# Performance work log

Hardware: AMD Instinct MI355X
Metric: run time of the kernel (lower is better)

Reference implementation:

```python
import jax, jax.numpy as jnp
import numpy as np
import math

B, N, C = 8, 2048, 512

def setup_inputs() -> dict:
    key = jax.random.key(0)
    ks = jax.random.split(key, 7)
    s = 1.0 / math.sqrt(C)
    return {
        "feature": jax.random.normal(ks[0], (B, N, C), dtype=jnp.float32),
        "wq": jax.random.uniform(ks[1], (C, C), jnp.float32, -s, s),
        "bq": jax.random.uniform(ks[2], (C,), jnp.float32, -s, s),
        "wk": jax.random.uniform(ks[3], (C, C), jnp.float32, -s, s),
        "bk": jax.random.uniform(ks[4], (C,), jnp.float32, -s, s),
        "wv": jax.random.uniform(ks[5], (C, C), jnp.float32, -s, s),
        "bv": jax.random.uniform(ks[6], (C,), jnp.float32, -s, s),
    }

def reference(feature, wq, bq, wk, bk, wv, bv):
    # torch nn.Linear: x @ W.T + b
    q = jnp.einsum('bnc,dc->bnd', feature, wq) + bq
    k = jnp.einsum('bnc,dc->bnd', feature, wk) + bk
    v = jnp.einsum('bnc,dc->bnd', feature, wv) + bv
    scores = jnp.einsum('bnd,bmd->bnm', q, k)          # [B, N, N]
    attn = jax.nn.softmax(scores, axis=2) / math.sqrt(C)  # post-softmax scale (as in source)
    v_star = jnp.einsum('bnm,bmd->bnd', attn, v)
    return feature + v_star
```

## Files before the change

### kernel.cpp

```cpp
#include <hip/hip_runtime.h>
#include <cstdint>
#include <cstddef>


typedef __bf16 bf16x8 __attribute__((ext_vector_type(8)));
typedef float f32x4 __attribute__((ext_vector_type(4)));
typedef float f32x16 __attribute__((ext_vector_type(16)));
typedef short short4v __attribute__((ext_vector_type(4)));
typedef short short8v __attribute__((ext_vector_type(8)));

__device__ __forceinline__ short f2b(float f) {
  union { float f; unsigned u; } u; u.f = f;
  unsigned r = (u.u + 0x7fffu + ((u.u >> 16) & 1u)) >> 16;
  return (short)r;
}

#define GLDS(gptr, lptr) \
  __builtin_amdgcn_global_load_lds( \
      (const __attribute__((address_space(1))) unsigned int*)(const void*)(gptr), \
      (__attribute__((address_space(3))) unsigned int*)(void*)(lptr), 16, 0, 0)

__device__ __forceinline__ bf16x8 ldfrag64(const short* buf, int row, int kq) {
  return *(const bf16x8*)(buf + row * 64 + ((kq ^ (row & 7)) * 8));
}

__global__ __launch_bounds__(256) void prep(const float* __restrict__ f,
                                            const float* __restrict__ w0,
                                            const float* __restrict__ w1,
                                            const float* __restrict__ w2,
                                            const float* __restrict__ b0,
                                            const float* __restrict__ b1,
                                            const float* __restrict__ b2,
                                            short* __restrict__ Xb, short* __restrict__ Wb,
                                            float* __restrict__ biasP, float* __restrict__ l) {
  const int bid = blockIdx.x;
  const int t = threadIdx.x;
  if (bid < 8192) {
    int i = bid * 256 + t;
    float4 v = ((const float4*)f)[i];
    short4v o = { f2b(v.x), f2b(v.y), f2b(v.z), f2b(v.w) };
    *(short4v*)(Xb + (size_t)i * 4) = o;
  } else if (bid < 8960) {
    int i = (bid - 8192) * 256 + t;
    const float* src = (i < 65536) ? w0 : (i < 131072) ? w1 : w2;
    float4 v = ((const float4*)src)[i & 65535];
    short4v o = { f2b(v.x), f2b(v.y), f2b(v.z), f2b(v.w) };
    *(short4v*)(Wb + (size_t)i * 4) = o;
  } else {
    int i = (bid - 8960) * 256 + t;
    float4 z = { 0.f, 0.f, 0.f, 0.f };
    ((float4*)l)[i * 2] = z;
    ((float4*)l)[i * 2 + 1] = z;
    if (i < 1536) {
      const float* s = (i < 512) ? b0 : (i < 1024) ? b1 : b2;
      biasP[i] = s[i & 511];
    }
  }
}

__global__ __launch_bounds__(256) void gemm_qkv(const short* __restrict__ X,
                                                const short* __restrict__ Wall,
                                                const float* __restrict__ biasP,
                                                short* __restrict__ Out,
                                                short* __restrict__ VtOut) {
  __shared__ __align__(16) short Xs[128 * 64];
  __shared__ __align__(16) short Ws[128 * 64];
  const int z = blockIdx.z;
  const short* Wm = Wall + (size_t)z * 262144;
  const int m0 = blockIdx.y * 128, n0 = blockIdx.x * 128;
  const int t = threadIdx.x;
  const int lane = t & 63, w = t >> 6;
  const int wn = (w & 1) * 64, wm = (w >> 1) * 64;
  const int fr = lane & 15, l4 = lane >> 4;

  f32x4 acc[4][4] = {};

  for (int k0 = 0; k0 < 512; k0 += 64) {
    __syncthreads();
#pragma unroll
    for (int u = 0; u < 4; ++u) {
      int cc = t + u * 256;
      int r = cc >> 3, cs = cc & 7;
      int kk = ((cs ^ (r & 7)) * 8);
      GLDS(X + (size_t)(m0 + r) * 512 + k0 + kk, Xs + cc * 8);
      GLDS(Wm + (size_t)(n0 + r) * 512 + k0 + kk, Ws + cc * 8);
    }
    __syncthreads();
#pragma unroll
    for (int h = 0; h < 2; ++h) {
      bf16x8 wf[4], xf[4];
#pragma unroll
      for (int i = 0; i < 4; ++i) wf[i] = ldfrag64(Ws, wn + i * 16 + fr, h * 4 + l4);
#pragma unroll
      for (int j = 0; j < 4; ++j) xf[j] = ldfrag64(Xs, wm + j * 16 + fr, h * 4 + l4);
      if (z < 2) {
#pragma unroll
        for (int i = 0; i < 4; ++i)
#pragma unroll
          for (int j = 0; j < 4; ++j)
            acc[i][j] = __builtin_amdgcn_mfma_f32_16x16x32_bf16(wf[i], xf[j], acc[i][j], 0, 0, 0);
      } else {
#pragma unroll
        for (int i = 0; i < 4; ++i)
#pragma unroll
          for (int j = 0; j < 4; ++j)
            acc[i][j] = __builtin_amdgcn_mfma_f32_16x16x32_bf16(xf[i], wf[j], acc[i][j], 0, 0, 0);
      }
    }
  }

  const int rq = l4 * 4;
  if (z < 2) {
#pragma unroll
    for (int i = 0; i < 4; ++i) {
      int nb = n0 + wn + i * 16 + rq;
      float4 bs = *(const float4*)(biasP + z * 512 + nb);
#pragma unroll
      for (int j = 0; j < 4; ++j) {
        int m = m0 + wm + j * 16 + fr;
        short4v o = { f2b(acc[i][j][0] + bs.x), f2b(acc[i][j][1] + bs.y),
                      f2b(acc[i][j][2] + bs.z), f2b(acc[i][j][3] + bs.w) };
        *(short4v*)(Out + (size_t)z * 8388608 + (size_t)m * 512 + nb) = o;
      }
    }
  } else {
    const int zB = blockIdx.y >> 4;
    const int mb = m0 & 2047;
#pragma unroll
    for (int j = 0; j < 4; ++j) {
      int d = n0 + wn + j * 16 + fr;
      float bd = biasP[1024 + d];
#pragma unroll
      for (int i = 0; i < 4; ++i) {
        int mloc = mb + wm + i * 16 + rq;
        short4v o = { f2b(acc[i][j][0] + bd), f2b(acc[i][j][1] + bd),
                      f2b(acc[i][j][2] + bd), f2b(acc[i][j][3] + bd) };
        *(short4v*)(VtOut + (size_t)zB * 1048576 + (size_t)d * 2048 + mloc) = o;
      }
    }
  }
}

__global__ __launch_bounds__(256) void gemm_qk(const short* __restrict__ Q,
                                               const short* __restrict__ Kb,
                                               short* __restrict__ P,
                                               float* __restrict__ l) {
  __shared__ __align__(16) short Qs[128 * 64];
  __shared__ __align__(16) short Ks[128 * 64];
  const int z = blockIdx.z;
  const short* A = Q + (size_t)z * 2048 * 512;
  const short* Bm = Kb + (size_t)z * 2048 * 512;
  const int m0 = blockIdx.y * 128, n0 = blockIdx.x * 128;
  const int t = threadIdx.x;
  const int lane = t & 63, w = t >> 6;
  const int wn = (w & 1) * 64, wm = (w >> 1) * 64;
  const int c31 = lane & 31, l5 = lane >> 5;

  f32x16 acc[2][2] = {};

  for (int k0 = 0; k0 < 512; k0 += 64) {
    __syncthreads();
#pragma unroll
    for (int u = 0; u < 4; ++u) {
      int cc = t + u * 256;
      int r = cc >> 3, cs = cc & 7;
      int kk = ((cs ^ (r & 7)) * 8);
      GLDS(A + (size_t)(m0 + r) * 512 + k0 + kk, Qs + cc * 8);
      GLDS(Bm + (size_t)(n0 + r) * 512 + k0 + kk, Ks + cc * 8);
    }
    __syncthreads();
#pragma unroll
    for (int ks = 0; ks < 4; ++ks) {
      const int kq = ks * 2 + l5;
      bf16x8 kf[2], qf[2];
#pragma unroll
      for (int i = 0; i < 2; ++i) kf[i] = ldfrag64(Ks, wn + i * 32 + c31, kq);
#pragma unroll
      for (int j = 0; j < 2; ++j) qf[j] = ldfrag64(Qs, wm + j * 32 + c31, kq);
#pragma unroll
      for (int i = 0; i < 2; ++i)
#pragma unroll
        for (int j = 0; j < 2; ++j)
          acc[i][j] = __builtin_amdgcn_mfma_f32_32x32x16_bf16(kf[i], qf[j], acc[i][j], 0, 0, 0);
    }
  }

  float rs[2] = { 0.f, 0.f };
#pragma unroll
  for (int i = 0; i < 2; ++i)
#pragma unroll
    for (int q = 0; q < 4; ++q) {
      int nb = n0 + wn + i * 32 + q * 8 + l5 * 4;
#pragma unroll
      for (int j = 0; j < 2; ++j) {
        int m = m0 + wm + j * 32 + c31;
        short4v o;
        float part = 0.f;
#pragma unroll
        for (int r = 0; r < 4; ++r) {
          float e = exp2f(acc[i][j][q * 4 + r] * 1.4426950408889634f);
          o[r] = f2b(e);
          part += e;
        }
        *(short4v*)(P + (size_t)z * 4194304 + (size_t)m * 2048 + nb) = o;
        rs[j] += part;
      }
    }
#pragma unroll
  for (int j = 0; j < 2; ++j) rs[j] += __shfl_xor(rs[j], 32);
  if (lane < 32) {
#pragma unroll
    for (int j = 0; j < 2; ++j)
      atomicAdd(&l[z * 2048 + m0 + wm + j * 32 + lane], rs[j]);
  }
}

__global__ __launch_bounds__(256) void gemm_pv(const short* __restrict__ Pm,
                                               const short* __restrict__ Vt,
                                               const float* __restrict__ l,
                                               const float* __restrict__ resid,
                                               float* __restrict__ out, float scale) {
  __shared__ __align__(16) short Ps[64 * 64];
  __shared__ __align__(16) short Vs[2][128 * 64];
  const int z = blockIdx.z;
  const short* A = Pm + (size_t)z * 4194304;
  const short* Bm = Vt + (size_t)z * 1048576;
  const int m0 = blockIdx.y * 64, n0 = blockIdx.x * 256;
  const int t = threadIdx.x;
  const int lane = t & 63, w = t >> 6;
  const int wn = (w & 1) * 64, wm = (w >> 1) * 32;
  const int c31 = lane & 31, l5 = lane >> 5;

  f32x16 acc[2][2] = {};

  for (int k0 = 0; k0 < 2048; k0 += 64) {
    __syncthreads();
#pragma unroll
    for (int u = 0; u < 2; ++u) {
      int cc = t + u * 256;
      int r = cc >> 3, cs = cc & 7;
      int kk = ((cs ^ (r & 7)) * 8);
      GLDS(A + (size_t)(m0 + r) * 2048 + k0 + kk, Ps + cc * 8);
    }
#pragma unroll
    for (int nt = 0; nt < 2; ++nt)
#pragma unroll
      for (int u = 0; u < 4; ++u) {
        int cc = t + u * 256;
        int r = cc >> 3, cs = cc & 7;
        int kk = ((cs ^ (r & 7)) * 8);
        GLDS(Bm + (size_t)(n0 + nt * 128 + r) * 2048 + k0 + kk, Vs[nt] + cc * 8);
      }
    __syncthreads();
#pragma unroll
    for (int ks = 0; ks < 4; ++ks) {
      const int kq = ks * 2 + l5;
      bf16x8 pf = ldfrag64(Ps, wm + c31, kq);
#pragma unroll
      for (int nt = 0; nt < 2; ++nt)
#pragma unroll
        for (int i = 0; i < 2; ++i) {
          bf16x8 vf = ldfrag64(Vs[nt], wn + i * 32 + c31, kq);
          acc[nt][i] = __builtin_amdgcn_mfma_f32_32x32x16_bf16(vf, pf, acc[nt][i], 0, 0, 0);
        }
    }
  }

  const int m = m0 + wm + c31;
  const float linv = scale / l[z * 2048 + m];
#pragma unroll
  for (int nt = 0; nt < 2; ++nt)
#pragma unroll
    for (int i = 0; i < 2; ++i)
#pragma unroll
      for (int q = 0; q < 4; ++q) {
        int d = n0 + nt * 128 + wn + i * 32 + q * 8 + l5 * 4;
        size_t idx = (size_t)z * 1048576 + (size_t)m * 512 + d;
        float4 rv = *(const float4*)(resid + idx);
        float4 o = { rv.x + acc[nt][i][q * 4 + 0] * linv, rv.y + acc[nt][i][q * 4 + 1] * linv,
                     rv.z + acc[nt][i][q * 4 + 2] * linv, rv.w + acc[nt][i][q * 4 + 3] * linv };
        *(float4*)(out + idx) = o;
      }
}

extern "C" void kernel_launch(void* const* d_in, const int* in_sizes, int n_in,
                              void* d_out, int out_size, void* d_ws, size_t ws_size,
                              hipStream_t stream) {
  const float* feature = (const float*)d_in[0];
  const float* wq = (const float*)d_in[1];
  const float* bq = (const float*)d_in[2];
  const float* wk = (const float*)d_in[3];
  const float* bk = (const float*)d_in[4];
  const float* wv = (const float*)d_in[5];
  const float* bv = (const float*)d_in[6];
  float* out = (float*)d_out;

  const size_t MN = (size_t)16384 * 512;
  short* Xb = (short*)d_ws;
  short* Wb = Xb + MN;
  short* Q = Wb + 786432;
  short* K = Q + MN;
  short* Vt = K + MN;
  short* P = Vt + MN;
  float* biasP = (float*)(P + (size_t)8 * 2048 * 2048);
  float* l = biasP + 1536;

  prep<<<8968, 256, 0, stream>>>(feature, wq, wk, wv, bq, bk, bv, Xb, Wb, biasP, l);

  gemm_qkv<<<dim3(4, 128, 3), 256, 0, stream>>>(Xb, Wb, biasP, Q, Vt);
  gemm_qk<<<dim3(16, 16, 8), 256, 0, stream>>>(Q, K, P, l);

  const float iscl = 0.044194173824159216f;
  gemm_pv<<<dim3(2, 32, 8), 256, 0, stream>>>(P, Vt, l, feature, out, iscl);
}
```

Baseline: 250.4 us.

## Rewrite QK and PV GEMMs as 8-wave 256-tiles with pipelined LDS loads

Replaces the QK^T and PV kernels with 512-thread versions that use 256x256 (QK) and 128x256 (PV) output tiles and 16x16x32 MFMA instructions. Global-to-LDS loads are double-buffered and interleaved with four compute phases per k-step, using explicit vmcnt waits, barriers and setprio. The intent is to hide global memory latency and raise data reuse per block, at the cost of more LDS per block and fragile hand-tuned wait counts. Operand roles are swapped so that keys and Vt form the A side.

Result: no change. 250.5 us (+0.0%).

```diff
diff --git a/kernel.cpp b/kernel.cpp
--- a/kernel.cpp
+++ b/kernel.cpp
@@ -5,9 +5,7 @@
 
 typedef __bf16 bf16x8 __attribute__((ext_vector_type(8)));
 typedef float f32x4 __attribute__((ext_vector_type(4)));
-typedef float f32x16 __attribute__((ext_vector_type(16)));
 typedef short short4v __attribute__((ext_vector_type(4)));
-typedef short short8v __attribute__((ext_vector_type(8)));
 
 __device__ __forceinline__ short f2b(float f) {
   union { float f; unsigned u; } u; u.f = f;
@@ -22,6 +20,53 @@
 
 __device__ __forceinline__ bf16x8 ldfrag64(const short* buf, int row, int kq) {
   return *(const bf16x8*)(buf + row * 64 + ((kq ^ (row & 7)) * 8));
+}
+
+template <int VM>
+__device__ __forceinline__ void ph_mid() {
+  if constexpr (VM >= 0) asm volatile("s_waitcnt vmcnt(%0)" ::"n"(VM) : "memory");
+  __builtin_amdgcn_s_barrier();
+  __builtin_amdgcn_s_setprio(1);
+}
+__device__ __forceinline__ void ph_end() {
+  __builtin_amdgcn_s_setprio(0);
+  __builtin_amdgcn_s_barrier();
+  __builtin_amdgcn_sched_barrier(0);
+}
+
+__device__ __forceinline__ void ldA4(bf16x8 (&a)[4][2], const short* buf, int rb, int l4) {
+#pragma unroll
+  for (int j = 0; j < 4; ++j)
+#pragma unroll
+    for (int kk = 0; kk < 2; ++kk) a[j][kk] = ldfrag64(buf, rb + j * 16, kk * 4 + l4);
+}
+__device__ __forceinline__ void ld2(bf16x8 (&b)[2][2], const short* buf, int rb, int l4) {
+#pragma unroll
+  for (int n = 0; n < 2; ++n)
+#pragma unroll
+    for (int kk = 0; kk < 2; ++kk) b[n][kk] = ldfrag64(buf, rb + n * 16, kk * 4 + l4);
+}
+__device__ __forceinline__ void mm42(f32x4 (&acc)[8][4], const bf16x8 (&a)[4][2],
+                                     const bf16x8 (&b)[2][2], int io, int no) {
+#pragma unroll
+  for (int j = 0; j < 4; ++j)
+#pragma unroll
+    for (int n = 0; n < 2; ++n)
+#pragma unroll
+      for (int kk = 0; kk < 2; ++kk)
+        acc[io + j][no + n] = __builtin_amdgcn_mfma_f32_16x16x32_bf16(
+            a[j][kk], b[n][kk], acc[io + j][no + n], 0, 0, 0);
+}
+__device__ __forceinline__ void mm22(f32x4 (&acc)[4][4], const bf16x8 (&a)[2][2],
+                                     const bf16x8 (&b)[2][2], int io, int no) {
+#pragma unroll
+  for (int j = 0; j < 2; ++j)
+#pragma unroll
+    for (int n = 0; n < 2; ++n)
+#pragma unroll
+      for (int kk = 0; kk < 2; ++kk)
+        acc[io + j][no + n] = __builtin_amdgcn_mfma_f32_16x16x32_bf16(
+            a[j][kk], b[n][kk], acc[io + j][no + n], 0, 0, 0);
 }
 
 __global__ __launch_bounds__(256) void prep(const float* __restrict__ f,
@@ -141,146 +186,212 @@
   }
 }
 
-__global__ __launch_bounds__(256) void gemm_qk(const short* __restrict__ Q,
-                                               const short* __restrict__ Kb,
-                                               short* __restrict__ P,
-                                               float* __restrict__ l) {
-  __shared__ __align__(16) short Qs[128 * 64];
-  __shared__ __align__(16) short Ks[128 * 64];
+__global__ __launch_bounds__(512, 2) void gemm_qk8(const short* __restrict__ Q,
+                                                   const short* __restrict__ Kb,
+                                                   short* __restrict__ P,
+                                                   float* __restrict__ l) {
+  __shared__ __align__(16) short As[2][16384];
+  __shared__ __align__(16) short Bs[2][16384];
   const int z = blockIdx.z;
-  const short* A = Q + (size_t)z * 2048 * 512;
-  const short* Bm = Kb + (size_t)z * 2048 * 512;
-  const int m0 = blockIdx.y * 128, n0 = blockIdx.x * 128;
+  const short* __restrict__ A = Kb + (size_t)z * 1048576;
+  const short* __restrict__ B = Q + (size_t)z * 1048576;
+  const int m0 = blockIdx.y * 256;
+  const int n0 = blockIdx.x * 256;
   const int t = threadIdx.x;
   const int lane = t & 63, w = t >> 6;
-  const int wn = (w & 1) * 64, wm = (w >> 1) * 64;
-  const int c31 = lane & 31, l5 = lane >> 5;
-
-  f32x16 acc[2][2] = {};
-
-  for (int k0 = 0; k0 < 512; k0 += 64) {
-    __syncthreads();
-#pragma unroll
-    for (int u = 0; u < 4; ++u) {
-      int cc = t + u * 256;
-      int r = cc >> 3, cs = cc & 7;
-      int kk = ((cs ^ (r & 7)) * 8);
-      GLDS(A + (size_t)(m0 + r) * 512 + k0 + kk, Qs + cc * 8);
-      GLDS(Bm + (size_t)(n0 + r) * 512 + k0 + kk, Ks + cc * 8);
-    }
-    __syncthreads();
-#pragma unroll
-    for (int ks = 0; ks < 4; ++ks) {
-      const int kq = ks * 2 + l5;
-      bf16x8 kf[2], qf[2];
-#pragma unroll
-      for (int i = 0; i < 2; ++i) kf[i] = ldfrag64(Ks, wn + i * 32 + c31, kq);
-#pragma unroll
-      for (int j = 0; j < 2; ++j) qf[j] = ldfrag64(Qs, wm + j * 32 + c31, kq);
-#pragma unroll
-      for (int i = 0; i < 2; ++i)
-#pragma unroll
-        for (int j = 0; j < 2; ++j)
-          acc[i][j] = __builtin_amdgcn_mfma_f32_32x32x16_bf16(kf[i], qf[j], acc[i][j], 0, 0, 0);
-    }
-  }
-
-  float rs[2] = { 0.f, 0.f };
-#pragma unroll
-  for (int i = 0; i < 2; ++i)
-#pragma unroll
-    for (int q = 0; q < 4; ++q) {
-      int nb = n0 + wn + i * 32 + q * 8 + l5 * 4;
-#pragma unroll
-      for (int j = 0; j < 2; ++j) {
-        int m = m0 + wm + j * 32 + c31;
-        short4v o;
-        float part = 0.f;
-#pragma unroll
-        for (int r = 0; r < 4; ++r) {
-          float e = exp2f(acc[i][j][q * 4 + r] * 1.4426950408889634f);
-          o[r] = f2b(e);
-          part += e;
-        }
-        *(short4v*)(P + (size_t)z * 4194304 + (size_t)m * 2048 + nb) = o;
-        rs[j] += part;
+  const int aw = (w >> 2) * 64, bw = (w & 3) * 32;
+  const int fr = lane & 15, l4 = lane >> 4;
+  const int r0 = t >> 3;
+  const int kswz = ((t & 7) ^ (r0 & 7)) * 8;
+  const short* pA = A + (size_t)(m0 + r0) * 512 + kswz;
+  const short* pB = B + (size_t)(n0 + r0) * 512 + kswz;
+
+#define QK_STG_A(buf, h, kt) do { \
+    GLDS(pA + (size_t)((h) * 128) * 512 + (kt) * 64, &As[(buf)][(h) * 8192 + t * 8]); \
+    GLDS(pA + (size_t)((h) * 128 + 64) * 512 + (kt) * 64, &As[(buf)][(h) * 8192 + 4096 + t * 8]); \
+  } while (0)
+#define QK_STG_B(buf, h, kt) do { \
+    GLDS(pB + (size_t)((h) * 128) * 512 + (kt) * 64, &Bs[(buf)][(h) * 8192 + t * 8]); \
+    GLDS(pB + (size_t)((h) * 128 + 64) * 512 + (kt) * 64, &Bs[(buf)][(h) * 8192 + 4096 + t * 8]); \
+  } while (0)
+
+  f32x4 acc[8][4] = {};
+
+  QK_STG_A(0, 0, 0); QK_STG_B(0, 0, 0); QK_STG_B(0, 1, 0); QK_STG_A(0, 1, 0);
+  QK_STG_A(1, 0, 1); QK_STG_B(1, 0, 1); QK_STG_B(1, 1, 1);
+  asm volatile("s_waitcnt vmcnt(10)" ::: "memory");
+  __builtin_amdgcn_s_barrier();
+  __builtin_amdgcn_sched_barrier(0);
+
+  bf16x8 af[4][2], b0[2][2], b1[2][2];
+  for (int kt = 0; kt < 6; ++kt) {
+    const int c = kt & 1;
+    const short* Ac = &As[c][0];
+    const short* Bc = &Bs[c][0];
+    ldA4(af, Ac, aw + fr, l4); ld2(b0, Bc, bw + fr, l4);
+    QK_STG_A(c ^ 1, 1, kt + 1);
+    ph_mid<10>(); mm42(acc, af, b0, 0, 0); ph_end();
+    ld2(b1, Bc, 128 + bw + fr, l4);
+    QK_STG_A(c, 0, kt + 2);
+    ph_mid<10>(); mm42(acc, af, b1, 0, 2); ph_end();
+    ldA4(af, Ac, 128 + aw + fr, l4);
+    QK_STG_B(c, 0, kt + 2);
+    ph_mid<-1>(); mm42(acc, af, b1, 4, 2); ph_end();
+    QK_STG_B(c, 1, kt + 2);
+    ph_mid<10>(); mm42(acc, af, b0, 4, 0); ph_end();
+  }
+  {
+    const short *Ac = &As[0][0], *Bc = &Bs[0][0];
+    ldA4(af, Ac, aw + fr, l4); ld2(b0, Bc, bw + fr, l4);
+    QK_STG_A(1, 1, 7);
+    ph_mid<10>(); mm42(acc, af, b0, 0, 0); ph_end();
+    ld2(b1, Bc, 128 + bw + fr, l4);
+    ph_mid<8>();  mm42(acc, af, b1, 0, 2); ph_end();
+    ldA4(af, Ac, 128 + aw + fr, l4);
+    ph_mid<-1>(); mm42(acc, af, b1, 4, 2); ph_end();
+    ph_mid<4>();  mm42(acc, af, b0, 4, 0); ph_end();
+  }
+  {
+    const short *Ac = &As[1][0], *Bc = &Bs[1][0];
+    ldA4(af, Ac, aw + fr, l4); ld2(b0, Bc, bw + fr, l4);
+    ph_mid<2>();  mm42(acc, af, b0, 0, 0); ph_end();
+    ld2(b1, Bc, 128 + bw + fr, l4);
+    ph_mid<0>();  mm42(acc, af, b1, 0, 2); ph_end();
+    ldA4(af, Ac, 128 + aw + fr, l4);
+    ph_mid<-1>(); mm42(acc, af, b1, 4, 2); ph_end();
+    ph_mid<-1>(); mm42(acc, af, b0, 4, 0); ph_end();
+  }
+#undef QK_STG_A
+#undef QK_STG_B
+
+  const float LOG2E = 1.4426950408889634f;
+  float rs[4] = { 0.f, 0.f, 0.f, 0.f };
+#pragma unroll
+  for (int i = 0; i < 8; ++i) {
+    const int key = m0 + aw + (i & 3) * 16 + (i >> 2) * 128 + l4 * 4;
+#pragma unroll
+    for (int n = 0; n < 4; ++n) {
+      const int q = n0 + bw + (n & 1) * 16 + (n >> 1) * 128 + fr;
+      short4v o;
+      float part = 0.f;
+#pragma unroll
+      for (int r = 0; r < 4; ++r) {
+        float e = exp2f(acc[i][n][r] * LOG2E);
+        o[r] = f2b(e);
+        part += e;
       }
-    }
-#pragma unroll
-  for (int j = 0; j < 2; ++j) rs[j] += __shfl_xor(rs[j], 32);
-  if (lane < 32) {
-#pragma unroll
-    for (int j = 0; j < 2; ++j)
-      atomicAdd(&l[z * 2048 + m0 + wm + j * 32 + lane], rs[j]);
-  }
-}
-
-__global__ __launch_bounds__(256) void gemm_pv(const short* __restrict__ Pm,
-                                               const short* __restrict__ Vt,
-                                               const float* __restrict__ l,
-                                               const float* __restrict__ resid,
-                                               float* __restrict__ out, float scale) {
-  __shared__ __align__(16) short Ps[64 * 64];
-  __shared__ __align__(16) short Vs[2][128 * 64];
+      *(short4v*)(P + (size_t)z * 4194304 + (size_t)q * 2048 + key) = o;
+      rs[n] += part;
+    }
+  }
+#pragma unroll
+  for (int n = 0; n < 4; ++n) {
+    rs[n] += __shfl_xor(rs[n], 16);
+    rs[n] += __shfl_xor(rs[n], 32);
+  }
+  if (l4 == 0) {
+#pragma unroll
+    for (int n = 0; n < 4; ++n)
+      atomicAdd(&l[z * 2048 + n0 + bw + (n & 1) * 16 + (n >> 1) * 128 + fr], rs[n]);
+  }
+}
+
+__global__ __launch_bounds__(512, 2) void gemm_pv8(const short* __restrict__ Pm,
+                                                   const short* __restrict__ Vt,
+                                                   const float* __restrict__ l,
+                                                   const float* __restrict__ resid,
+                                                   float* __restrict__ out, float scale) {
+  __shared__ __align__(16) short As[2][8192];
+  __shared__ __align__(16) short Bs[2][16384];
   const int z = blockIdx.z;
-  const short* A = Pm + (size_t)z * 4194304;
-  const short* Bm = Vt + (size_t)z * 1048576;
-  const int m0 = blockIdx.y * 64, n0 = blockIdx.x * 256;
+  const short* __restrict__ A = Vt + (size_t)z * 1048576;
+  const short* __restrict__ B = Pm + (size_t)z * 4194304;
+  const int d0 = blockIdx.x * 128;
+  const int n0 = blockIdx.y * 256;
   const int t = threadIdx.x;
   const int lane = t & 63, w = t >> 6;
-  const int wn = (w & 1) * 64, wm = (w >> 1) * 32;
-  const int c31 = lane & 31, l5 = lane >> 5;
-
-  f32x16 acc[2][2] = {};
-
-  for (int k0 = 0; k0 < 2048; k0 += 64) {
-    __syncthreads();
-#pragma unroll
-    for (int u = 0; u < 2; ++u) {
-      int cc = t + u * 256;
-      int r = cc >> 3, cs = cc & 7;
-      int kk = ((cs ^ (r & 7)) * 8);
-      GLDS(A + (size_t)(m0 + r) * 2048 + k0 + kk, Ps + cc * 8);
-    }
-#pragma unroll
-    for (int nt = 0; nt < 2; ++nt)
-#pragma unroll
-      for (int u = 0; u < 4; ++u) {
-        int cc = t + u * 256;
-        int r = cc >> 3, cs = cc & 7;
-        int kk = ((cs ^ (r & 7)) * 8);
-        GLDS(Bm + (size_t)(n0 + nt * 128 + r) * 2048 + k0 + kk, Vs[nt] + cc * 8);
-      }
-    __syncthreads();
-#pragma unroll
-    for (int ks = 0; ks < 4; ++ks) {
-      const int kq = ks * 2 + l5;
-      bf16x8 pf = ldfrag64(Ps, wm + c31, kq);
-#pragma unroll
-      for (int nt = 0; nt < 2; ++nt)
-#pragma unroll
-        for (int i = 0; i < 2; ++i) {
-          bf16x8 vf = ldfrag64(Vs[nt], wn + i * 32 + c31, kq);
-          acc[nt][i] = __builtin_amdgcn_mfma_f32_32x32x16_bf16(vf, pf, acc[nt][i], 0, 0, 0);
-        }
-    }
-  }
-
-  const int m = m0 + wm + c31;
-  const float linv = scale / l[z * 2048 + m];
-#pragma unroll
-  for (int nt = 0; nt < 2; ++nt)
-#pragma unroll
-    for (int i = 0; i < 2; ++i)
-#pragma unroll
-      for (int q = 0; q < 4; ++q) {
-        int d = n0 + nt * 128 + wn + i * 32 + q * 8 + l5 * 4;
-        size_t idx = (size_t)z * 1048576 + (size_t)m * 512 + d;
-        float4 rv = *(const float4*)(resid + idx);
-        float4 o = { rv.x + acc[nt][i][q * 4 + 0] * linv, rv.y + acc[nt][i][q * 4 + 1] * linv,
-                     rv.z + acc[nt][i][q * 4 + 2] * linv, rv.w + acc[nt][i][q * 4 + 3] * linv };
-        *(float4*)(out + idx) = o;
-      }
+  const int aw = (w >> 2) * 32, bw = (w & 3) * 32;
+  const int fr = lane & 15, l4 = lane >> 4;
+  const int r0 = t >> 3;
+  const int kswz = ((t & 7) ^ (r0 & 7)) * 8;
+  const short* pA = A + (size_t)(d0 + r0) * 2048 + kswz;
+  const short* pB = B + (size_t)(n0 + r0) * 2048 + kswz;
+
+#define PV_STG_A(buf, h, kt) \
+    GLDS(pA + (size_t)((h) * 64) * 2048 + (kt) * 64, &As[(buf)][(h) * 4096 + t * 8])
+#define PV_STG_B(buf, h, kt) do { \
+    GLDS(pB + (size_t)((h) * 128) * 2048 + (kt) * 64, &Bs[(buf)][(h) * 8192 + t * 8]); \
+    GLDS(pB + (size_t)((h) * 128 + 64) * 2048 + (kt) * 64, &Bs[(buf)][(h) * 8192 + 4096 + t * 8]); \
+  } while (0)
+
+  f32x4 acc[4][4] = {};
+
+  PV_STG_A(0, 0, 0); PV_STG_B(0, 0, 0); PV_STG_B(0, 1, 0); PV_STG_A(0, 1, 0);
+  PV_STG_A(1, 0, 1); PV_STG_B(1, 0, 1); PV_STG_B(1, 1, 1);
+  asm volatile("s_waitcnt vmcnt(8)" ::: "memory");
+  __builtin_amdgcn_s_barrier();
+  __builtin_amdgcn_sched_barrier(0);
+
+  bf16x8 a[2][2], b0[2][2], b1[2][2];
+  for (int kt = 0; kt < 30; ++kt) {
+    const int c = kt & 1;
+    const short* Ac = &As[c][0];
+    const short* Bc = &Bs[c][0];
+    ld2(a, Ac, aw + fr, l4); ld2(b0, Bc, bw + fr, l4);
+    PV_STG_A(c ^ 1, 1, kt + 1);
+    ph_mid<7>(); mm22(acc, a, b0, 0, 0); ph_end();
+    ld2(b1, Bc, 128 + bw + fr, l4);
+    PV_STG_A(c, 0, kt + 2);
+    ph_mid<7>(); mm22(acc, a, b1, 0, 2); ph_end();
+    ld2(a, Ac, 64 + aw + fr, l4);
+    PV_STG_B(c, 0, kt + 2);
+    ph_mid<-1>(); mm22(acc, a, b1, 2, 2); ph_end();
+    PV_STG_B(c, 1, kt + 2);
+    ph_mid<8>(); mm22(acc, a, b0, 2, 0); ph_end();
+  }
+  {
+    const short *Ac = &As[0][0], *Bc = &Bs[0][0];
+    ld2(a, Ac, aw + fr, l4); ld2(b0, Bc, bw + fr, l4);
+    PV_STG_A(1, 1, 31);
+    ph_mid<7>(); mm22(acc, a, b0, 0, 0); ph_end();
+    ld2(b1, Bc, 128 + bw + fr, l4);
+    ph_mid<6>(); mm22(acc, a, b1, 0, 2); ph_end();
+    ld2(a, Ac, 64 + aw + fr, l4);
+    ph_mid<-1>(); mm22(acc, a, b1, 2, 2); ph_end();
+    ph_mid<3>(); mm22(acc, a, b0, 2, 0); ph_end();
+  }
+  {
+    const short *Ac = &As[1][0], *Bc = &Bs[1][0];
+    ld2(a, Ac, aw + fr, l4); ld2(b0, Bc, bw + fr, l4);
+    ph_mid<1>(); mm22(acc, a, b0, 0, 0); ph_end();
+    ld2(b1, Bc, 128 + bw + fr, l4);
+    ph_mid<0>(); mm22(acc, a, b1, 0, 2); ph_end();
+    ld2(a, Ac, 64 + aw + fr, l4);
+    ph_mid<-1>(); mm22(acc, a, b1, 2, 2); ph_end();
+    ph_mid<-1>(); mm22(acc, a, b0, 2, 0); ph_end();
+  }
+#undef PV_STG_A
+#undef PV_STG_B
+
+  float linv[4];
+#pragma unroll
+  for (int n = 0; n < 4; ++n) {
+    const int q = n0 + bw + (n & 1) * 16 + (n >> 1) * 128 + fr;
+    linv[n] = scale / l[z * 2048 + q];
+  }
+#pragma unroll
+  for (int n = 0; n < 4; ++n) {
+    const int q = n0 + bw + (n & 1) * 16 + (n >> 1) * 128 + fr;
+#pragma unroll
+    for (int i = 0; i < 4; ++i) {
+      const int d = d0 + aw + (i & 1) * 16 + (i >> 1) * 64 + l4 * 4;
+      const size_t idx = (size_t)z * 1048576 + (size_t)q * 512 + d;
+      float4 rv = *(const float4*)(resid + idx);
+      float4 o = { rv.x + acc[i][n][0] * linv[n], rv.y + acc[i][n][1] * linv[n],
+                   rv.z + acc[i][n][2] * linv[n], rv.w + acc[i][n][3] * linv[n] };
+      *(float4*)(out + idx) = o;
+    }
+  }
 }
 
 extern "C" void kernel_launch(void* const* d_in, const int* in_sizes, int n_in,
@@ -308,8 +419,8 @@
   prep<<<8968, 256, 0, stream>>>(feature, wq, wk, wv, bq, bk, bv, Xb, Wb, biasP, l);
 
   gemm_qkv<<<dim3(4, 128, 3), 256, 0, stream>>>(Xb, Wb, biasP, Q, Vt);
-  gemm_qk<<<dim3(16, 16, 8), 256, 0, stream>>>(Q, K, P, l);
+  gemm_qk8<<<dim3(8, 8, 8), 512, 0, stream>>>(Q, K, P, l);
 
   const float iscl = 0.044194173824159216f;
-  gemm_pv<<<dim3(2, 32, 8), 256, 0, stream>>>(P, Vt, l, feature, out, iscl);
-}
+  gemm_pv8<<<dim3(4, 8, 8), 512, 0, stream>>>(P, Vt, l, feature, out, iscl);
+}
```

## Rewrite QK and PV GEMMs with double-buffered LDS pipeline and 16x16 MFMA

Applied to the files above, without the earlier changes.

Replaces the QK^T and PV kernels with versions that double-buffer LDS tiles of K-depth 32 and keep the next tile's global-to-LDS loads in flight using explicit vmcnt waits. The block-sized syncthreads pairs become raw barriers, and the MFMA sections run at raised wave priority. Both kernels switch from 32x32x16 to 16x16x32 MFMA with 4x4 accumulator tiles, and block IDs are swizzled for better cache locality. PV now uses 128x128 output tiles. The goal is to hide global-memory latency behind MFMA work, at the cost of more synchronisation points per K step and reliance on hand-placed waitcnt correctness.

Result: faster. 238.3 us (-4.8%).

```diff
diff --git a/kernel.cpp b/kernel.cpp
--- a/kernel.cpp
+++ b/kernel.cpp
@@ -5,9 +5,7 @@
 
 typedef __bf16 bf16x8 __attribute__((ext_vector_type(8)));
 typedef float f32x4 __attribute__((ext_vector_type(4)));
-typedef float f32x16 __attribute__((ext_vector_type(16)));
 typedef short short4v __attribute__((ext_vector_type(4)));
-typedef short short8v __attribute__((ext_vector_type(8)));
 
 __device__ __forceinline__ short f2b(float f) {
   union { float f; unsigned u; } u; u.f = f;
@@ -23,6 +21,23 @@
 __device__ __forceinline__ bf16x8 ldfrag64(const short* buf, int row, int kq) {
   return *(const bf16x8*)(buf + row * 64 + ((kq ^ (row & 7)) * 8));
 }
+
+__device__ __forceinline__ bf16x8 ldfrag32(const short* buf, int row, int l4) {
+  const short* p = buf + row * 32 + ((l4 ^ ((row >> 1) & 3)) * 8);
+  bf16x8 r;
+  asm volatile("ds_read_b128 %0, %1"
+               : "=v"(r)
+               : "v"((const __attribute__((address_space(3))) short*)(const void*)p));
+  return r;
+}
+
+#define LGKM0_SB() do { \
+    asm volatile("s_waitcnt lgkmcnt(0)" ::: "memory"); \
+    __builtin_amdgcn_sched_barrier(0); } while (0)
+#define VMW(n) asm volatile("s_waitcnt vmcnt(" #n ")" ::: "memory")
+#define SBAR() __builtin_amdgcn_s_barrier()
+#define PRIO1() __builtin_amdgcn_s_setprio(1)
+#define PRIO0() __builtin_amdgcn_s_setprio(0)
 
 __global__ __launch_bounds__(256) void prep(const float* __restrict__ f,
                                             const float* __restrict__ w0,
@@ -141,146 +156,166 @@
   }
 }
 
-__global__ __launch_bounds__(256) void gemm_qk(const short* __restrict__ Q,
-                                               const short* __restrict__ Kb,
-                                               short* __restrict__ P,
-                                               float* __restrict__ l) {
-  __shared__ __align__(16) short Qs[128 * 64];
-  __shared__ __align__(16) short Ks[128 * 64];
-  const int z = blockIdx.z;
-  const short* A = Q + (size_t)z * 2048 * 512;
-  const short* Bm = Kb + (size_t)z * 2048 * 512;
-  const int m0 = blockIdx.y * 128, n0 = blockIdx.x * 128;
+__global__ __launch_bounds__(256) void gemm_qk8(const short* __restrict__ Q,
+                                                const short* __restrict__ Kb,
+                                                short* __restrict__ P,
+                                                float* __restrict__ l) {
+  __shared__ __align__(16) short As[2][4096];
+  __shared__ __align__(16) short Bs[2][4096];
+  const int id = blockIdx.x + blockIdx.y * 16 + blockIdx.z * 256;
+  const int swz = (id & 7) * 256 + (id >> 3);
+  const int z = swz >> 8;
+  const int m0 = (swz & 15) * 128;
+  const int n0 = ((swz >> 4) & 15) * 128;
+  const short* __restrict__ A = Kb + (size_t)z * 1048576;
+  const short* __restrict__ B = Q + (size_t)z * 1048576;
   const int t = threadIdx.x;
   const int lane = t & 63, w = t >> 6;
-  const int wn = (w & 1) * 64, wm = (w >> 1) * 64;
-  const int c31 = lane & 31, l5 = lane >> 5;
-
-  f32x16 acc[2][2] = {};
-
-  for (int k0 = 0; k0 < 512; k0 += 64) {
-    __syncthreads();
-#pragma unroll
-    for (int u = 0; u < 4; ++u) {
-      int cc = t + u * 256;
-      int r = cc >> 3, cs = cc & 7;
-      int kk = ((cs ^ (r & 7)) * 8);
-      GLDS(A + (size_t)(m0 + r) * 512 + k0 + kk, Qs + cc * 8);
-      GLDS(Bm + (size_t)(n0 + r) * 512 + k0 + kk, Ks + cc * 8);
-    }
-    __syncthreads();
-#pragma unroll
-    for (int ks = 0; ks < 4; ++ks) {
-      const int kq = ks * 2 + l5;
-      bf16x8 kf[2], qf[2];
-#pragma unroll
-      for (int i = 0; i < 2; ++i) kf[i] = ldfrag64(Ks, wn + i * 32 + c31, kq);
-#pragma unroll
-      for (int j = 0; j < 2; ++j) qf[j] = ldfrag64(Qs, wm + j * 32 + c31, kq);
-#pragma unroll
-      for (int i = 0; i < 2; ++i)
-#pragma unroll
-        for (int j = 0; j < 2; ++j)
-          acc[i][j] = __builtin_amdgcn_mfma_f32_32x32x16_bf16(kf[i], qf[j], acc[i][j], 0, 0, 0);
-    }
-  }
-
-  float rs[2] = { 0.f, 0.f };
-#pragma unroll
-  for (int i = 0; i < 2; ++i)
-#pragma unroll
-    for (int q = 0; q < 4; ++q) {
-      int nb = n0 + wn + i * 32 + q * 8 + l5 * 4;
-#pragma unroll
-      for (int j = 0; j < 2; ++j) {
-        int m = m0 + wm + j * 32 + c31;
-        short4v o;
-        float part = 0.f;
-#pragma unroll
-        for (int r = 0; r < 4; ++r) {
-          float e = exp2f(acc[i][j][q * 4 + r] * 1.4426950408889634f);
-          o[r] = f2b(e);
-          part += e;
-        }
-        *(short4v*)(P + (size_t)z * 4194304 + (size_t)m * 2048 + nb) = o;
-        rs[j] += part;
+  const int aw = (w >> 1) * 64, bw = (w & 1) * 64;
+  const int fr = lane & 15, l4 = lane >> 4;
+  const int r0 = t >> 2, cs = t & 3;
+  const int csw = (cs ^ ((r0 >> 1) & 3)) * 8;
+  const short* pA = A + (size_t)(m0 + r0) * 512 + csw;
+  const short* pB = B + (size_t)(n0 + r0) * 512 + csw;
+
+#define QK_STG(buf, kt) do { \
+    GLDS(pA + (kt) * 32, &As[(buf)][t * 8]); \
+    GLDS(pA + 64 * 512 + (kt) * 32, &As[(buf)][2048 + t * 8]); \
+    GLDS(pB + (kt) * 32, &Bs[(buf)][t * 8]); \
+    GLDS(pB + 64 * 512 + (kt) * 32, &Bs[(buf)][2048 + t * 8]); \
+  } while (0)
+
+  f32x4 acc[4][4] = {};
+  bf16x8 a[4], b[4];
+
+  QK_STG(0, 0); QK_STG(1, 1);
+
+#pragma unroll 1
+  for (int kt = 0; kt < 16; ++kt) {
+    const int c = kt & 1;
+    if (kt >= 1 && kt < 15) QK_STG(c ^ 1, kt + 1);
+    if (kt < 15) { VMW(4); } else { VMW(0); }
+    SBAR();
+#pragma unroll
+    for (int i = 0; i < 4; ++i) a[i] = ldfrag32(&As[c][0], aw + i * 16 + fr, l4);
+#pragma unroll
+    for (int n = 0; n < 4; ++n) b[n] = ldfrag32(&Bs[c][0], bw + n * 16 + fr, l4);
+    LGKM0_SB(); PRIO1();
+#pragma unroll
+    for (int i = 0; i < 4; ++i)
+#pragma unroll
+      for (int n = 0; n < 4; ++n)
+        acc[i][n] = __builtin_amdgcn_mfma_f32_16x16x32_bf16(a[i], b[n], acc[i][n], 0, 0, 0);
+    PRIO0(); SBAR();
+  }
+#undef QK_STG
+
+  const float LOG2E = 1.4426950408889634f;
+  float rs[4] = { 0.f, 0.f, 0.f, 0.f };
+#pragma unroll
+  for (int i = 0; i < 4; ++i) {
+    const int key = m0 + aw + i * 16 + l4 * 4;
+#pragma unroll
+    for (int n = 0; n < 4; ++n) {
+      const int q = n0 + bw + n * 16 + fr;
+      short4v o;
+      float part = 0.f;
+#pragma unroll
+      for (int r = 0; r < 4; ++r) {
+        float e = exp2f(acc[i][n][r] * LOG2E);
+        o[r] = f2b(e);
+        part += e;
       }
-    }
-#pragma unroll
-  for (int j = 0; j < 2; ++j) rs[j] += __shfl_xor(rs[j], 32);
-  if (lane < 32) {
-#pragma unroll
-    for (int j = 0; j < 2; ++j)
-      atomicAdd(&l[z * 2048 + m0 + wm + j * 32 + lane], rs[j]);
-  }
-}
-
-__global__ __launch_bounds__(256) void gemm_pv(const short* __restrict__ Pm,
-                                               const short* __restrict__ Vt,
-                                               const float* __restrict__ l,
-                                               const float* __restrict__ resid,
-                                               float* __restrict__ out, float scale) {
-  __shared__ __align__(16) short Ps[64 * 64];
-  __shared__ __align__(16) short Vs[2][128 * 64];
-  const int z = blockIdx.z;
-  const short* A = Pm + (size_t)z * 4194304;
-  const short* Bm = Vt + (size_t)z * 1048576;
-  const int m0 = blockIdx.y * 64, n0 = blockIdx.x * 256;
+      *(short4v*)(P + (size_t)z * 4194304 + (size_t)q * 2048 + key) = o;
+      rs[n] += part;
+    }
+  }
+#pragma unroll
+  for (int n = 0; n < 4; ++n) {
+    rs[n] += __shfl_xor(rs[n], 16);
+    rs[n] += __shfl_xor(rs[n], 32);
+  }
+  if (l4 == 0) {
+#pragma unroll
+    for (int n = 0; n < 4; ++n)
+      atomicAdd(&l[z * 2048 + n0 + bw + n * 16 + fr], rs[n]);
+  }
+}
+
+__global__ __launch_bounds__(256) void gemm_pv8(const short* __restrict__ Pm,
+                                                const short* __restrict__ Vt,
+                                                const float* __restrict__ l,
+                                                const float* __restrict__ resid,
+                                                float* __restrict__ out, float scale) {
+  __shared__ __align__(16) short As[2][4096];
+  __shared__ __align__(16) short Bs[2][4096];
+  const int id = blockIdx.x + blockIdx.y * 4 + blockIdx.z * 64;
+  const int swz = (id & 7) * 64 + (id >> 3);
+  const int z = swz >> 6;
+  const int d0 = (swz & 3) * 128;
+  const int n0 = ((swz >> 2) & 15) * 128;
+  const short* __restrict__ A = Vt + (size_t)z * 1048576;
+  const short* __restrict__ B = Pm + (size_t)z * 4194304;
   const int t = threadIdx.x;
   const int lane = t & 63, w = t >> 6;
-  const int wn = (w & 1) * 64, wm = (w >> 1) * 32;
-  const int c31 = lane & 31, l5 = lane >> 5;
-
-  f32x16 acc[2][2] = {};
-
-  for (int k0 = 0; k0 < 2048; k0 += 64) {
-    __syncthreads();
-#pragma unroll
-    for (int u = 0; u < 2; ++u) {
-      int cc = t + u * 256;
-      int r = cc >> 3, cs = cc & 7;
-      int kk = ((cs ^ (r & 7)) * 8);
-      GLDS(A + (size_t)(m0 + r) * 2048 + k0 + kk, Ps + cc * 8);
-    }
-#pragma unroll
-    for (int nt = 0; nt < 2; ++nt)
-#pragma unroll
-      for (int u = 0; u < 4; ++u) {
-        int cc = t + u * 256;
-        int r = cc >> 3, cs = cc & 7;
-        int kk = ((cs ^ (r & 7)) * 8);
-        GLDS(Bm + (size_t)(n0 + nt * 128 + r) * 2048 + k0 + kk, Vs[nt] + cc * 8);
-      }
-    __syncthreads();
-#pragma unroll
-    for (int ks = 0; ks < 4; ++ks) {
-      const int kq = ks * 2 + l5;
-      bf16x8 pf = ldfrag64(Ps, wm + c31, kq);
-#pragma unroll
-      for (int nt = 0; nt < 2; ++nt)
-#pragma unroll
-        for (int i = 0; i < 2; ++i) {
-          bf16x8 vf = ldfrag64(Vs[nt], wn + i * 32 + c31, kq);
-          acc[nt][i] = __builtin_amdgcn_mfma_f32_32x32x16_bf16(vf, pf, acc[nt][i], 0, 0, 0);
-        }
-    }
-  }
-
-  const int m = m0 + wm + c31;
-  const float linv = scale / l[z * 2048 + m];
-#pragma unroll
-  for (int nt = 0; nt < 2; ++nt)
-#pragma unroll
-    for (int i = 0; i < 2; ++i)
-#pragma unroll
-      for (int q = 0; q < 4; ++q) {
-        int d = n0 + nt * 128 + wn + i * 32 + q * 8 + l5 * 4;
-        size_t idx = (size_t)z * 1048576 + (size_t)m * 512 + d;
-        float4 rv = *(const float4*)(resid + idx);
-        float4 o = { rv.x + acc[nt][i][q * 4 + 0] * linv, rv.y + acc[nt][i][q * 4 + 1] * linv,
-                     rv.z + acc[nt][i][q * 4 + 2] * linv, rv.w + acc[nt][i][q * 4 + 3] * linv };
-        *(float4*)(out + idx) = o;
-      }
+  const int aw = (w >> 1) * 64, bw = (w & 1) * 64;
+  const int fr = lane & 15, l4 = lane >> 4;
+  const int r0 = t >> 2, cs = t & 3;
+  const int csw = (cs ^ ((r0 >> 1) & 3)) * 8;
+  const short* pA = A + (size_t)(d0 + r0) * 2048 + csw;
+  const short* pB = B + (size_t)(n0 + r0) * 2048 + csw;
+
+#define PV_STG(buf, kt) do { \
+    GLDS(pA + (kt) * 32, &As[(buf)][t * 8]); \
+    GLDS(pA + (size_t)64 * 2048 + (kt) * 32, &As[(buf)][2048 + t * 8]); \
+    GLDS(pB + (kt) * 32, &Bs[(buf)][t * 8]); \
+    GLDS(pB + (size_t)64 * 2048 + (kt) * 32, &Bs[(buf)][2048 + t * 8]); \
+  } while (0)
+
+  f32x4 acc[4][4] = {};
+  bf16x8 a[4], b[4];
+
+  PV_STG(0, 0); PV_STG(1, 1);
+
+#pragma unroll 1
+  for (int kt = 0; kt < 64; ++kt) {
+    const int c = kt & 1;
+    if (kt >= 1 && kt < 63) PV_STG(c ^ 1, kt + 1);
+    if (kt < 63) { VMW(4); } else { VMW(0); }
+    SBAR();
+#pragma unroll
+    for (int i = 0; i < 4; ++i) a[i] = ldfrag32(&As[c][0], aw + i * 16 + fr, l4);
+#pragma unroll
+    for (int n = 0; n < 4; ++n) b[n] = ldfrag32(&Bs[c][0], bw + n * 16 + fr, l4);
+    LGKM0_SB(); PRIO1();
+#pragma unroll
+    for (int i = 0; i < 4; ++i)
+#pragma unroll
+      for (int n = 0; n < 4; ++n)
+        acc[i][n] = __builtin_amdgcn_mfma_f32_16x16x32_bf16(a[i], b[n], acc[i][n], 0, 0, 0);
+    PRIO0(); SBAR();
+  }
+#undef PV_STG
+
+  float linv[4];
+#pragma unroll
+  for (int n = 0; n < 4; ++n) {
+    const int q = n0 + bw + n * 16 + fr;
+    linv[n] = scale / l[z * 2048 + q];
+  }
+#pragma unroll
+  for (int n = 0; n < 4; ++n) {
+    const int q = n0 + bw + n * 16 + fr;
+#pragma unroll
+    for (int i = 0; i < 4; ++i) {
+      const int d = d0 + aw + i * 16 + l4 * 4;
+      const size_t idx = (size_t)z * 1048576 + (size_t)q * 512 + d;
+      float4 rv = *(const float4*)(resid + idx);
+      float4 o = { rv.x + acc[i][n][0] * linv[n], rv.y + acc[i][n][1] * linv[n],
+                   rv.z + acc[i][n][2] * linv[n], rv.w + acc[i][n][3] * linv[n] };
+      *(float4*)(out + idx) = o;
+    }
+  }
 }
 
 extern "C" void kernel_launch(void* const* d_in, const int* in_sizes, int n_in,
@@ -308,8 +343,8 @@
   prep<<<8968, 256, 0, stream>>>(feature, wq, wk, wv, bq, bk, bv, Xb, Wb, biasP, l);
 
   gemm_qkv<<<dim3(4, 128, 3), 256, 0, stream>>>(Xb, Wb, biasP, Q, Vt);
-  gemm_qk<<<dim3(16, 16, 8), 256, 0, stream>>>(Q, K, P, l);
+  gemm_qk8<<<dim3(16, 16, 8), 256, 0, stream>>>(Q, K, P, l);
 
   const float iscl = 0.044194173824159216f;
-  gemm_pv<<<dim3(2, 32, 8), 256, 0, stream>>>(P, Vt, l, feature, out, iscl);
-}
+  gemm_pv8<<<dim3(4, 16, 8), 256, 0, stream>>>(P, Vt, l, feature, out, iscl);
+}
```
